# Performance work log

Hardware: AMD Instinct MI355X
Metric: run time of the kernel (lower is better)

The kernel has to match this reference:

```python
import jax, jax.numpy as jnp
import numpy as np

B, T, D = 16, 4096, 512
V = 512          # cif value dim
H_ALPHA = 128    # alpha_net hidden
N_MAX = 400      # static max target length (fill_max of target_lengths)
EPS = 1e-8


def _layernorm(x, g, b, eps=1e-5):
    mu = jnp.mean(x, axis=-1, keepdims=True)
    var = jnp.mean(jnp.square(x - mu), axis=-1, keepdims=True)
    return (x - mu) * jax.lax.rsqrt(var + eps) * g + b


def setup_inputs() -> dict:
    key = jax.random.key(0)
    ks = jax.random.split(key, 10)
    h = jax.random.normal(ks[0], (B, T, D), dtype=jnp.float32)
    target_lengths = jax.random.randint(ks[1], (B,), 1, N_MAX + 1)          # 1..400
    input_lengths = jax.random.randint(ks[2], (B,), T // 2, T + 1)          # 2048..4096
    s = 1.0 / np.sqrt(D)
    params = {
        "ln_g": jnp.ones((D,), jnp.float32),
        "ln_b": jnp.zeros((D,), jnp.float32),
        "W1": jax.random.normal(ks[3], (D, H_ALPHA), jnp.float32) * s,
        "b1": jnp.zeros((H_ALPHA,), jnp.float32),
        "W2": jax.random.normal(ks[4], (H_ALPHA, 1), jnp.float32) * (1.0 / np.sqrt(H_ALPHA)),
        "b2": jnp.zeros((1,), jnp.float32),
        "Wv": jax.random.normal(ks[5], (D, V), jnp.float32) * s,
        "bv": jnp.zeros((V,), jnp.float32),
    }
    return {"h": h, "target_lengths": target_lengths, "input_lengths": input_lengths, **params}


def reference(h, target_lengths, input_lengths, ln_g, ln_b, W1, b1, W2, b2, Wv, bv):
    dt = h.dtype
    # alpha_net: LayerNorm -> Linear -> SiLU -> Linear -> softplus -> [B,T]
    x = _layernorm(h, ln_g, ln_b)
    x = jax.nn.silu(x @ W1 + b1)
    raw_alpha = jax.nn.softplus((x @ W2 + b2)[..., 0])  # [B,T]

    # mask padding & rescale so sum_t alpha = N per sample
    mask = (jnp.arange(T)[None, :] < input_lengths[:, None]).astype(dt)  # [B,T]
    alpha = raw_alpha * mask
    sums = jnp.sum(alpha, axis=1)                       # [B]
    Nf = target_lengths.astype(dt)
    alpha_scaled = alpha * (Nf / (sums + EPS))[:, None]
    Lf = jnp.maximum(input_lengths.astype(dt), 1.0)
    alpha_uniform = mask * (Nf / Lf)[:, None]
    use_uniform = (sums < 10 * EPS).astype(dt)[:, None]
    alpha = alpha_scaled * (1.0 - use_uniform) + alpha_uniform * use_uniform

    v = h @ Wv + bv                                     # [B,T,V]

    # mass-space overlap: w[b,t,k] = clamp(min(c_t,k) - max(c_{t-1},k-1), 0)
    c = jnp.cumsum(alpha, axis=1)                       # [B,T]
    c_prev = c - alpha
    k = jnp.arange(1, N_MAX + 1, dtype=dt)[None, None, :]  # [1,1,N]
    left = jnp.maximum(c_prev[..., None], k - 1.0)
    right = jnp.minimum(c[..., None], k)
    w = jnp.clip(right - left, 0.0)                     # [B,T,N]

    token_mask = jnp.arange(N_MAX)[None, :] < target_lengths[:, None]  # [B,N] bool
    tokens = jnp.einsum('btn,btv->bnv', w, v)           # [B,N,V]
    cif_mass = jnp.sum(w, axis=1)                       # [B,N]
    frame_durations = jnp.sum(w / (alpha + EPS)[..., None], axis=1)    # [B,N]

    tm = token_mask.astype(dt)
    tokens = tokens * tm[..., None]
    cif_mass = cif_mass * tm
    frame_durations = frame_durations * tm
    return tokens, frame_durations, cif_mass, token_mask, alpha, raw_alpha
```

## Files before the change

kernel.cpp:

```cpp
#include <hip/hip_runtime.h>
#include <math.h>


#define T_LEN 4096
#define D_DIM 512
#define HID   128
#define N_MAX 400
#define B_SZ  16
#define EPSF  1e-8f

typedef __attribute__((ext_vector_type(8))) short bf16x8;
typedef __attribute__((ext_vector_type(4))) float f32x4;

__device__ __forceinline__ unsigned short f2bf(float x) {
    unsigned u = __float_as_uint(x);
    unsigned r = (u + 0x7FFFu + ((u >> 16) & 1u)) >> 16;
    return (unsigned short)r;
}
__device__ __forceinline__ float bf2f(unsigned short h) {
    return __uint_as_float(((unsigned)h) << 16);
}

__global__ __launch_bounds__(256) void transpose_split_kernel(
    const float* __restrict__ in, unsigned short* __restrict__ out_hi,
    unsigned short* __restrict__ out_lo, int K, int N)
{
    __shared__ float tile[64][65];
    const int tid = threadIdx.x;
    const int k0 = blockIdx.x * 64, n0 = blockIdx.y * 64;
    #pragma unroll
    for (int i = 0; i < 16; ++i) {
        int idx = tid + i * 256;
        tile[idx >> 6][idx & 63] = in[(size_t)(k0 + (idx >> 6)) * N + n0 + (idx & 63)];
    }
    __syncthreads();
    #pragma unroll
    for (int i = 0; i < 16; ++i) {
        int idx = tid + i * 256;
        int nr = idx >> 6, kc = idx & 63;
        float x = tile[kc][nr];
        unsigned short hi = f2bf(x);
        out_hi[(size_t)(n0 + nr) * K + k0 + kc] = hi;
        if (out_lo) out_lo[(size_t)(n0 + nr) * K + k0 + kc] = f2bf(x - bf2f(hi));
    }
}

__global__ __launch_bounds__(256) void alpha_net_kernel(
    const float* __restrict__ h,
    const float* __restrict__ ln_g, const float* __restrict__ ln_b,
    const unsigned short* __restrict__ W1t_hi, const unsigned short* __restrict__ W1t_lo,
    const float* __restrict__ b1,
    const float* __restrict__ W2,   const float* __restrict__ b2,
    float* __restrict__ raw_alpha)
{
    __shared__ char planes[32 * 2064];
    __shared__ float part2[2][2][16];
    const int tid  = threadIdx.x;
    const int row0 = blockIdx.x * 32;
    const int wave = tid >> 6;
    const int lane = tid & 63;

    const int c1 = lane * 4;
    const int c2 = 256 + lane * 4;
    float4 g1 = *(const float4*)&ln_g[c1];
    float4 g2 = *(const float4*)&ln_g[c2];
    float4 o1 = *(const float4*)&ln_b[c1];
    float4 o2 = *(const float4*)&ln_b[c2];
    float4 av[8], bv8[8];
    const int rbase8 = wave * 8;
    #pragma unroll
    for (int rr = 0; rr < 8; ++rr) {
        const float* hrow = h + (size_t)(row0 + rbase8 + rr) * D_DIM;
        float4 a  = *(const float4*)(hrow + c1);
        float4 bq = *(const float4*)(hrow + c2);
        float s  = a.x + a.y + a.z + a.w + bq.x + bq.y + bq.z + bq.w;
        float sq = a.x*a.x + a.y*a.y + a.z*a.z + a.w*a.w
                 + bq.x*bq.x + bq.y*bq.y + bq.z*bq.z + bq.w*bq.w;
        #pragma unroll
        for (int off = 32; off >= 1; off >>= 1) {
            s  += __shfl_xor(s,  off);
            sq += __shfl_xor(sq, off);
        }
        float mu  = s * (1.0f / 512.0f);
        float var = sq * (1.0f / 512.0f) - mu * mu;
        float inv = rsqrtf(var + 1e-5f);
        a.x  = (a.x  - mu) * inv * g1.x + o1.x;
        a.y  = (a.y  - mu) * inv * g1.y + o1.y;
        a.z  = (a.z  - mu) * inv * g1.z + o1.z;
        a.w  = (a.w  - mu) * inv * g1.w + o1.w;
        bq.x = (bq.x - mu) * inv * g2.x + o2.x;
        bq.y = (bq.y - mu) * inv * g2.y + o2.y;
        bq.z = (bq.z - mu) * inv * g2.z + o2.z;
        bq.w = (bq.w - mu) * inv * g2.w + o2.w;
        av[rr] = a; bv8[rr] = bq;
    }
    #pragma unroll
    for (int rr = 0; rr < 8; ++rr) {
        char* rb = planes + (rbase8 + rr) * 2064;
        float4 a = av[rr], bq = bv8[rr];
        ushort4 ha = make_ushort4(f2bf(a.x), f2bf(a.y), f2bf(a.z), f2bf(a.w));
        ushort4 hb = make_ushort4(f2bf(bq.x), f2bf(bq.y), f2bf(bq.z), f2bf(bq.w));
        ushort4 la = make_ushort4(f2bf(a.x - bf2f(ha.x)), f2bf(a.y - bf2f(ha.y)),
                                  f2bf(a.z - bf2f(ha.z)), f2bf(a.w - bf2f(ha.w)));
        ushort4 lb = make_ushort4(f2bf(bq.x - bf2f(hb.x)), f2bf(bq.y - bf2f(hb.y)),
                                  f2bf(bq.z - bf2f(hb.z)), f2bf(bq.w - bf2f(hb.w)));
        *(ushort4*)(rb + 2 * c1)        = ha;
        *(ushort4*)(rb + 2 * c2)        = hb;
        *(ushort4*)(rb + 1024 + 2 * c1) = la;
        *(ushort4*)(rb + 1024 + 2 * c2) = lb;
    }
    __syncthreads();

    const int rt = wave >> 1, ch = wave & 1;
    const int lr = lane & 15, lg = lane >> 4;
    const char* aBase = planes + (rt * 16 + lr) * 2064;
    f32x4 acc[4];
    #pragma unroll
    for (int nt = 0; nt < 4; ++nt) acc[nt] = (f32x4){0.f, 0.f, 0.f, 0.f};
    for (int ks = 0; ks < 16; ++ks) {
        const int cofs = (4 * ks + lg) * 16;
        bf16x8 ahi = *(const bf16x8*)(aBase + cofs);
        bf16x8 alo = *(const bf16x8*)(aBase + 1024 + cofs);
        const int kofs = ks * 32 + lg * 8;
        #pragma unroll
        for (int nt = 0; nt < 4; ++nt) {
            int n = ch * 64 + nt * 16 + lr;
            bf16x8 bhi = *(const bf16x8*)(W1t_hi + (size_t)n * D_DIM + kofs);
            bf16x8 blo = *(const bf16x8*)(W1t_lo + (size_t)n * D_DIM + kofs);
            acc[nt] = __builtin_amdgcn_mfma_f32_16x16x32_bf16(ahi, bhi, acc[nt], 0, 0, 0);
            acc[nt] = __builtin_amdgcn_mfma_f32_16x16x32_bf16(ahi, blo, acc[nt], 0, 0, 0);
            acc[nt] = __builtin_amdgcn_mfma_f32_16x16x32_bf16(alo, bhi, acc[nt], 0, 0, 0);
        }
    }

    float p[4] = {0.f, 0.f, 0.f, 0.f};
    #pragma unroll
    for (int nt = 0; nt < 4; ++nt) {
        int n = ch * 64 + nt * 16 + lr;
        float b1v = b1[n], w2v = W2[n];
        #pragma unroll
        for (int j = 0; j < 4; ++j) {
            float z = acc[nt][j] + b1v;
            p[j] += z / (1.f + expf(-z)) * w2v;
        }
    }
    #pragma unroll
    for (int j = 0; j < 4; ++j) {
        p[j] += __shfl_xor(p[j], 1);
        p[j] += __shfl_xor(p[j], 2);
        p[j] += __shfl_xor(p[j], 4);
        p[j] += __shfl_xor(p[j], 8);
    }
    if (lr == 0) {
        #pragma unroll
        for (int j = 0; j < 4; ++j) part2[ch][rt][lg * 4 + j] = p[j];
    }
    __syncthreads();
    if (tid < 32) {
        int r16 = tid & 15, rt2 = tid >> 4;
        float z = part2[0][rt2][r16] + part2[1][rt2][r16] + b2[0];
        float sp = fmaxf(z, 0.f) + log1pf(expf(-fabsf(z)));
        raw_alpha[row0 + rt2 * 16 + r16] = sp;
    }
}

__global__ __launch_bounds__(256) void chunk_sum_kernel(
    const float* __restrict__ raw, const int* __restrict__ ilen,
    float* __restrict__ S)
{
    __shared__ float wred[4];
    const int ch = blockIdx.x, b = blockIdx.y;
    const int tid = threadIdx.x;
    const int L = min(ilen[b], T_LEN);
    const int base = ch << 10;
    float local = 0.f;
    #pragma unroll
    for (int i = 0; i < 4; ++i) {
        int t = base + tid + (i << 8);
        if (t < L) local += raw[b * T_LEN + t];
    }
    #pragma unroll
    for (int off = 32; off >= 1; off >>= 1) local += __shfl_xor(local, off);
    if ((tid & 63) == 0) wred[tid >> 6] = local;
    __syncthreads();
    if (tid == 0) S[b * 4 + ch] = wred[0] + wred[1] + wred[2] + wred[3];
}

__global__ __launch_bounds__(1024) void scan_chunk_kernel(
    const float* __restrict__ raw, const float* __restrict__ S,
    const int* __restrict__ tgt, const int* __restrict__ ilen,
    float* __restrict__ alpha_out, float* __restrict__ c_out)
{
    __shared__ float wsum_lds[16];
    __shared__ float wscan_lds[16];
    const int ch = blockIdx.x, b = blockIdx.y;
    const int tid  = threadIdx.x;
    const int wid  = tid >> 6;
    const int lane = tid & 63;
    const int L    = min(ilen[b], T_LEN);
    const float Nf = (float)tgt[b];

    float s0 = S[b * 4 + 0], s1 = S[b * 4 + 1], s2 = S[b * 4 + 2], s3 = S[b * 4 + 3];
    float sums  = s0 + s1 + s2 + s3;
    float scale = Nf / (sums + EPSF);
    float uu    = (sums < 10.f * EPSF) ? 1.f : 0.f;
    float unif  = Nf / fmaxf((float)L, 1.f);
    float prefix = (ch > 0 ? s0 : 0.f) + (ch > 1 ? s1 : 0.f) + (ch > 2 ? s2 : 0.f);
    float carry  = (1.f - uu) * scale * prefix
                 + uu * unif * (float)min(L, ch << 10);

    int t = (ch << 10) + tid;
    float m = (t < L) ? 1.f : 0.f;
    float a = (raw[b * T_LEN + t] * m * scale) * (1.f - uu) + m * unif * uu;
    alpha_out[b * T_LEN + t] = a;

    float v = a;
    #pragma unroll
    for (int off = 1; off < 64; off <<= 1) {
        float tv = __shfl_up(v, off);
        if (lane >= off) v += tv;
    }
    if (lane == 63) wsum_lds[wid] = v;
    __syncthreads();
    if (wid == 0 && lane < 16) {
        float s = wsum_lds[lane];
        #pragma unroll
        for (int off = 1; off < 16; off <<= 1) {
            float tv = __shfl_up(s, off);
            if (lane >= off) s += tv;
        }
        wscan_lds[lane] = s;
    }
    __syncthreads();
    float woff = (wid > 0) ? wscan_lds[wid - 1] : 0.f;
    c_out[b * T_LEN + t] = carry + woff + v;
}

__global__ __launch_bounds__(256) void cif_gather_kernel(
    const float* __restrict__ h, const float* __restrict__ alpha,
    const float* __restrict__ c_arr,
    const int* __restrict__ tgt, const int* __restrict__ ilen,
    unsigned short* __restrict__ hwb, float* __restrict__ fd_out,
    float* __restrict__ cm_out, float* __restrict__ tm_out)
{
    __shared__ float part[514];
    const int n   = blockIdx.x;
    const int b   = blockIdx.y;
    const int tid = threadIdx.x;
    const int oidx = b * N_MAX + n;
    if (n >= tgt[b]) {
        if (tid == 0) { fd_out[oidx] = 0.f; cm_out[oidx] = 0.f; tm_out[oidx] = 0.f; }
        return;
    }
    const int L = min(ilen[b], T_LEN);
    const float* cb = c_arr + b * T_LEN;
    const float* ab = alpha + b * T_LEN;
    const float nf  = (float)n;
    const float nf1 = nf + 1.0f;

    int lo = 0, hi = T_LEN;
    while (lo < hi) { int mid = (lo + hi) >> 1; if (cb[mid] > nf) hi = mid; else lo = mid + 1; }
    const int t0 = lo;
    lo = 0; hi = T_LEN;
    while (lo < hi) { int mid = (lo + hi) >> 1; if (cb[mid] >= nf1) hi = mid; else lo = mid + 1; }
    int t1 = min(lo, L - 1);

    const int par = tid >> 7;
    const int c4  = (tid & 127) << 2;
    float4 acc = make_float4(0.f, 0.f, 0.f, 0.f);
    float wsum = 0.f, fdsum = 0.f;
    const float* hb = h + (size_t)(b * T_LEN) * D_DIM;
    for (int t = t0 + par; t <= t1; t += 2) {
        float a = ab[t], c = cb[t];
        float cp = c - a;
        float w  = fmaxf(fminf(c, nf1) - fmaxf(cp, nf), 0.f);
        wsum  += w;
        fdsum += w / (a + EPSF);
        const float4 hv = *(const float4*)(hb + (size_t)t * D_DIM + c4);
        acc.x += w * hv.x;
        acc.y += w * hv.y;
        acc.z += w * hv.z;
        acc.w += w * hv.w;
    }
    if (par == 1) {
        *(float4*)&part[c4] = acc;
        if (tid == 128) { part[512] = wsum; part[513] = fdsum; }
    }
    __syncthreads();
    if (par == 0) {
        float4 p = *(const float4*)&part[c4];
        acc.x += p.x; acc.y += p.y; acc.z += p.z; acc.w += p.w;
        *(ushort4*)(hwb + (size_t)oidx * D_DIM + c4) =
            make_ushort4(f2bf(acc.x), f2bf(acc.y), f2bf(acc.z), f2bf(acc.w));
        if (tid == 0) {
            fd_out[oidx] = fdsum + part[513];
            cm_out[oidx] = wsum + part[512];
            tm_out[oidx] = 1.f;
        }
    }
}

__global__ __launch_bounds__(256) void token_gemm_kernel(
    const unsigned short* __restrict__ hwb, const unsigned short* __restrict__ Wvt,
    const float* __restrict__ bv, const float* __restrict__ cm,
    const int* __restrict__ tgt, float* __restrict__ tokens)
{
    const int tid  = threadIdx.x;
    const int wave = tid >> 6;
    const int lane = tid & 63;
    const int lr = lane & 15, lg = lane >> 4;
    const int arow = blockIdx.x * 64 + wave * 16 + lr;
    const int colb = blockIdx.y * 128;

    f32x4 acc[8];
    #pragma unroll
    for (int nt = 0; nt < 8; ++nt) acc[nt] = (f32x4){0.f, 0.f, 0.f, 0.f};
    for (int ks = 0; ks < 16; ++ks) {
        const int kofs = ks * 32 + lg * 8;
        bf16x8 a = *(const bf16x8*)(hwb + (size_t)arow * D_DIM + kofs);
        #pragma unroll
        for (int nt = 0; nt < 8; ++nt) {
            int n = colb + nt * 16 + lr;
            bf16x8 bq = *(const bf16x8*)(Wvt + (size_t)n * D_DIM + kofs);
            acc[nt] = __builtin_amdgcn_mfma_f32_16x16x32_bf16(a, bq, acc[nt], 0, 0, 0);
        }
    }

    float cmr[4], mr[4];
    int   rr[4];
    #pragma unroll
    for (int j = 0; j < 4; ++j) {
        int r = blockIdx.x * 64 + wave * 16 + lg * 4 + j;
        int bb = r / N_MAX;
        int nn = r - bb * N_MAX;
        rr[j] = r;
        mr[j] = (nn < tgt[bb]) ? 1.f : 0.f;
        cmr[j] = cm[r];
    }
    #pragma unroll
    for (int nt = 0; nt < 8; ++nt) {
        int col = colb + nt * 16 + lr;
        float bvv = bv[col];
        #pragma unroll
        for (int j = 0; j < 4; ++j)
            tokens[(size_t)rr[j] * D_DIM + col] = mr[j] * (acc[nt][j] + cmr[j] * bvv);
    }
}

extern "C" void kernel_launch(void* const* d_in, const int* in_sizes, int n_in,
                              void* d_out, int out_size, void* d_ws, size_t ws_size,
                              hipStream_t stream)
{
    (void)in_sizes; (void)n_in; (void)out_size; (void)ws_size;
    const float* h    = (const float*)d_in[0];
    const int*   tgt  = (const int*)  d_in[1];
    const int*   ilen = (const int*)  d_in[2];
    const float* lng  = (const float*)d_in[3];
    const float* lnb  = (const float*)d_in[4];
    const float* W1   = (const float*)d_in[5];
    const float* b1   = (const float*)d_in[6];
    const float* W2   = (const float*)d_in[7];
    const float* b2   = (const float*)d_in[8];
    const float* Wv   = (const float*)d_in[9];
    const float* bv   = (const float*)d_in[10];

    float* out    = (float*)d_out;
    float* tokens = out;
    float* fd     = tokens + (size_t)B_SZ * N_MAX * D_DIM;
    float* cm     = fd + B_SZ * N_MAX;
    float* tm     = cm + B_SZ * N_MAX;
    float* alpha  = tm + B_SZ * N_MAX;
    float* raw    = alpha + B_SZ * T_LEN;

    float* c_ws = (float*)d_ws;
    unsigned short* hwb    = (unsigned short*)(c_ws + B_SZ * T_LEN);
    unsigned short* W1t_hi = hwb + (size_t)B_SZ * N_MAX * D_DIM;
    unsigned short* W1t_lo = W1t_hi + (size_t)HID * D_DIM;
    unsigned short* Wvt    = W1t_lo + (size_t)HID * D_DIM;
    float* S = (float*)(Wvt + (size_t)D_DIM * D_DIM);

    transpose_split_kernel<<<dim3(8, 2), 256, 0, stream>>>(W1, W1t_hi, W1t_lo, D_DIM, HID);
    transpose_split_kernel<<<dim3(8, 8), 256, 0, stream>>>(Wv, Wvt, (unsigned short*)nullptr,
                                                           D_DIM, D_DIM);
    alpha_net_kernel<<<(B_SZ * T_LEN) / 32, 256, 0, stream>>>(h, lng, lnb, W1t_hi, W1t_lo,
                                                              b1, W2, b2, raw);
    chunk_sum_kernel<<<dim3(4, B_SZ), 256, 0, stream>>>(raw, ilen, S);
    scan_chunk_kernel<<<dim3(4, B_SZ), 1024, 0, stream>>>(raw, S, tgt, ilen, alpha, c_ws);
    cif_gather_kernel<<<dim3(N_MAX, B_SZ), 256, 0, stream>>>(h, alpha, c_ws, tgt, ilen,
                                                             hwb, fd, cm, tm);
    token_gemm_kernel<<<dim3(100, 4), 256, 0, stream>>>(hwb, Wvt, bv, cm, tgt, tokens);
}
```

Before: 410.3 us.

## Pack weights into MFMA fragment order and rebalance alpha-net wave tiling

Replaces the shared-memory weight transpose with a kernel that writes W1 and Wv directly in per-lane MFMA fragment order, so each wave's B-operand load becomes one contiguous 16-byte-per-lane access. In alpha_net, each wave now computes both 16-row tiles over 32 hidden columns instead of one row tile over 64 columns. This halves how much weight data each wave reads and reuses the A fragments held in registers. The layernorm and bf16-split stores are also fused into a single loop, dropping the register arrays. The pack kernel reads the weights with strided global loads, but it runs only once per call on small matrices.

```diff
diff --git a/kernel.cpp b/kernel.cpp
--- a/kernel.cpp
+++ b/kernel.cpp
@@ -21,40 +21,45 @@
     return __uint_as_float(((unsigned)h) << 16);
 }
 
-__global__ __launch_bounds__(256) void transpose_split_kernel(
+__global__ __launch_bounds__(256) void frag_pack_kernel(
     const float* __restrict__ in, unsigned short* __restrict__ out_hi,
     unsigned short* __restrict__ out_lo, int K, int N)
 {
-    __shared__ float tile[64][65];
-    const int tid = threadIdx.x;
-    const int k0 = blockIdx.x * 64, n0 = blockIdx.y * 64;
-    #pragma unroll
-    for (int i = 0; i < 16; ++i) {
-        int idx = tid + i * 256;
-        tile[idx >> 6][idx & 63] = in[(size_t)(k0 + (idx >> 6)) * N + n0 + (idx & 63)];
-    }
-    __syncthreads();
-    #pragma unroll
-    for (int i = 0; i < 16; ++i) {
-        int idx = tid + i * 256;
-        int nr = idx >> 6, kc = idx & 63;
-        float x = tile[kc][nr];
+    const int idx = blockIdx.x * 256 + threadIdx.x;
+    const int nks = K >> 5;
+    const int total = (N >> 4) * nks * 64;
+    if (idx >= total) return;
+    const int lane = idx & 63;
+    const int ks   = (idx >> 6) % nks;
+    const int ntg  = idx / (nks << 6);
+    const int n  = ntg * 16 + (lane & 15);
+    const int k0 = ks * 32 + (lane >> 4) * 8;
+    unsigned short hv[8], lv[8];
+    #pragma unroll
+    for (int e = 0; e < 8; ++e) {
+        float x = in[(size_t)(k0 + e) * N + n];
         unsigned short hi = f2bf(x);
-        out_hi[(size_t)(n0 + nr) * K + k0 + kc] = hi;
-        if (out_lo) out_lo[(size_t)(n0 + nr) * K + k0 + kc] = f2bf(x - bf2f(hi));
+        hv[e] = hi;
+        lv[e] = f2bf(x - bf2f(hi));
+    }
+    *(ushort4*)(out_hi + (size_t)idx * 8)     = make_ushort4(hv[0], hv[1], hv[2], hv[3]);
+    *(ushort4*)(out_hi + (size_t)idx * 8 + 4) = make_ushort4(hv[4], hv[5], hv[6], hv[7]);
+    if (out_lo) {
+        *(ushort4*)(out_lo + (size_t)idx * 8)     = make_ushort4(lv[0], lv[1], lv[2], lv[3]);
+        *(ushort4*)(out_lo + (size_t)idx * 8 + 4) = make_ushort4(lv[4], lv[5], lv[6], lv[7]);
     }
 }
 
 __global__ __launch_bounds__(256) void alpha_net_kernel(
     const float* __restrict__ h,
     const float* __restrict__ ln_g, const float* __restrict__ ln_b,
-    const unsigned short* __restrict__ W1t_hi, const unsigned short* __restrict__ W1t_lo,
+    const unsigned short* __restrict__ W1f_hi, const unsigned short* __restrict__ W1f_lo,
     const float* __restrict__ b1,
     const float* __restrict__ W2,   const float* __restrict__ b2,
     float* __restrict__ raw_alpha)
 {
     __shared__ char planes[32 * 2064];
-    __shared__ float part2[2][2][16];
+    __shared__ float part2[4][2][16];
     const int tid  = threadIdx.x;
     const int row0 = blockIdx.x * 32;
     const int wave = tid >> 6;
@@ -66,7 +71,6 @@
     float4 g2 = *(const float4*)&ln_g[c2];
     float4 o1 = *(const float4*)&ln_b[c1];
     float4 o2 = *(const float4*)&ln_b[c2];
-    float4 av[8], bv8[8];
     const int rbase8 = wave * 8;
     #pragma unroll
     for (int rr = 0; rr < 8; ++rr) {
@@ -92,12 +96,7 @@
         bq.y = (bq.y - mu) * inv * g2.y + o2.y;
         bq.z = (bq.z - mu) * inv * g2.z + o2.z;
         bq.w = (bq.w - mu) * inv * g2.w + o2.w;
-        av[rr] = a; bv8[rr] = bq;
-    }
-    #pragma unroll
-    for (int rr = 0; rr < 8; ++rr) {
         char* rb = planes + (rbase8 + rr) * 2064;
-        float4 a = av[rr], bq = bv8[rr];
         ushort4 ha = make_ushort4(f2bf(a.x), f2bf(a.y), f2bf(a.z), f2bf(a.w));
         ushort4 hb = make_ushort4(f2bf(bq.x), f2bf(bq.y), f2bf(bq.z), f2bf(bq.w));
         ushort4 la = make_ushort4(f2bf(a.x - bf2f(ha.x)), f2bf(a.y - bf2f(ha.y)),
@@ -111,54 +110,67 @@
     }
     __syncthreads();
 
-    const int rt = wave >> 1, ch = wave & 1;
     const int lr = lane & 15, lg = lane >> 4;
-    const char* aBase = planes + (rt * 16 + lr) * 2064;
-    f32x4 acc[4];
-    #pragma unroll
-    for (int nt = 0; nt < 4; ++nt) acc[nt] = (f32x4){0.f, 0.f, 0.f, 0.f};
+    const char* aBase0 = planes + lr * 2064;
+    const char* aBase1 = planes + (16 + lr) * 2064;
+    f32x4 acc[2][2];
+    #pragma unroll
+    for (int rt = 0; rt < 2; ++rt)
+        #pragma unroll
+        for (int nt = 0; nt < 2; ++nt) acc[rt][nt] = (f32x4){0.f, 0.f, 0.f, 0.f};
     for (int ks = 0; ks < 16; ++ks) {
         const int cofs = (4 * ks + lg) * 16;
-        bf16x8 ahi = *(const bf16x8*)(aBase + cofs);
-        bf16x8 alo = *(const bf16x8*)(aBase + 1024 + cofs);
-        const int kofs = ks * 32 + lg * 8;
-        #pragma unroll
-        for (int nt = 0; nt < 4; ++nt) {
-            int n = ch * 64 + nt * 16 + lr;
-            bf16x8 bhi = *(const bf16x8*)(W1t_hi + (size_t)n * D_DIM + kofs);
-            bf16x8 blo = *(const bf16x8*)(W1t_lo + (size_t)n * D_DIM + kofs);
-            acc[nt] = __builtin_amdgcn_mfma_f32_16x16x32_bf16(ahi, bhi, acc[nt], 0, 0, 0);
-            acc[nt] = __builtin_amdgcn_mfma_f32_16x16x32_bf16(ahi, blo, acc[nt], 0, 0, 0);
-            acc[nt] = __builtin_amdgcn_mfma_f32_16x16x32_bf16(alo, bhi, acc[nt], 0, 0, 0);
-        }
-    }
-
-    float p[4] = {0.f, 0.f, 0.f, 0.f};
-    #pragma unroll
-    for (int nt = 0; nt < 4; ++nt) {
-        int n = ch * 64 + nt * 16 + lr;
+        bf16x8 ahi0 = *(const bf16x8*)(aBase0 + cofs);
+        bf16x8 alo0 = *(const bf16x8*)(aBase0 + 1024 + cofs);
+        bf16x8 ahi1 = *(const bf16x8*)(aBase1 + cofs);
+        bf16x8 alo1 = *(const bf16x8*)(aBase1 + 1024 + cofs);
+        #pragma unroll
+        for (int nt = 0; nt < 2; ++nt) {
+            const size_t fo = ((size_t)((wave * 2 + nt) * 16 + ks) * 64 + lane) * 8;
+            bf16x8 bhi = *(const bf16x8*)(W1f_hi + fo);
+            bf16x8 blo = *(const bf16x8*)(W1f_lo + fo);
+            acc[0][nt] = __builtin_amdgcn_mfma_f32_16x16x32_bf16(ahi0, bhi, acc[0][nt], 0, 0, 0);
+            acc[0][nt] = __builtin_amdgcn_mfma_f32_16x16x32_bf16(ahi0, blo, acc[0][nt], 0, 0, 0);
+            acc[0][nt] = __builtin_amdgcn_mfma_f32_16x16x32_bf16(alo0, bhi, acc[0][nt], 0, 0, 0);
+            acc[1][nt] = __builtin_amdgcn_mfma_f32_16x16x32_bf16(ahi1, bhi, acc[1][nt], 0, 0, 0);
+            acc[1][nt] = __builtin_amdgcn_mfma_f32_16x16x32_bf16(ahi1, blo, acc[1][nt], 0, 0, 0);
+            acc[1][nt] = __builtin_amdgcn_mfma_f32_16x16x32_bf16(alo1, bhi, acc[1][nt], 0, 0, 0);
+        }
+    }
+
+    float p[2][4] = {};
+    #pragma unroll
+    for (int nt = 0; nt < 2; ++nt) {
+        int n = (wave * 2 + nt) * 16 + lr;
         float b1v = b1[n], w2v = W2[n];
         #pragma unroll
+        for (int rt = 0; rt < 2; ++rt)
+            #pragma unroll
+            for (int j = 0; j < 4; ++j) {
+                float z = acc[rt][nt][j] + b1v;
+                p[rt][j] += z / (1.f + expf(-z)) * w2v;
+            }
+    }
+    #pragma unroll
+    for (int rt = 0; rt < 2; ++rt)
+        #pragma unroll
         for (int j = 0; j < 4; ++j) {
-            float z = acc[nt][j] + b1v;
-            p[j] += z / (1.f + expf(-z)) * w2v;
-        }
-    }
-    #pragma unroll
-    for (int j = 0; j < 4; ++j) {
-        p[j] += __shfl_xor(p[j], 1);
-        p[j] += __shfl_xor(p[j], 2);
-        p[j] += __shfl_xor(p[j], 4);
-        p[j] += __shfl_xor(p[j], 8);
-    }
+            p[rt][j] += __shfl_xor(p[rt][j], 1);
+            p[rt][j] += __shfl_xor(p[rt][j], 2);
+            p[rt][j] += __shfl_xor(p[rt][j], 4);
+            p[rt][j] += __shfl_xor(p[rt][j], 8);
+        }
     if (lr == 0) {
         #pragma unroll
-        for (int j = 0; j < 4; ++j) part2[ch][rt][lg * 4 + j] = p[j];
+        for (int rt = 0; rt < 2; ++rt)
+            #pragma unroll
+            for (int j = 0; j < 4; ++j) part2[wave][rt][lg * 4 + j] = p[rt][j];
     }
     __syncthreads();
     if (tid < 32) {
         int r16 = tid & 15, rt2 = tid >> 4;
-        float z = part2[0][rt2][r16] + part2[1][rt2][r16] + b2[0];
+        float z = part2[0][rt2][r16] + part2[1][rt2][r16]
+                + part2[2][rt2][r16] + part2[3][rt2][r16] + b2[0];
         float sp = fmaxf(z, 0.f) + log1pf(expf(-fabsf(z)));
         raw_alpha[row0 + rt2 * 16 + r16] = sp;
     }
@@ -301,7 +313,7 @@
 }
 
 __global__ __launch_bounds__(256) void token_gemm_kernel(
-    const unsigned short* __restrict__ hwb, const unsigned short* __restrict__ Wvt,
+    const unsigned short* __restrict__ hwb, const unsigned short* __restrict__ Wvf,
     const float* __restrict__ bv, const float* __restrict__ cm,
     const int* __restrict__ tgt, float* __restrict__ tokens)
 {
@@ -320,8 +332,8 @@
         bf16x8 a = *(const bf16x8*)(hwb + (size_t)arow * D_DIM + kofs);
         #pragma unroll
         for (int nt = 0; nt < 8; ++nt) {
-            int n = colb + nt * 16 + lr;
-            bf16x8 bq = *(const bf16x8*)(Wvt + (size_t)n * D_DIM + kofs);
+            const int ntg = blockIdx.y * 8 + nt;
+            bf16x8 bq = *(const bf16x8*)(Wvf + ((size_t)(ntg * 16 + ks) * 64 + lane) * 8);
             acc[nt] = __builtin_amdgcn_mfma_f32_16x16x32_bf16(a, bq, acc[nt], 0, 0, 0);
         }
     }
@@ -374,19 +386,18 @@
 
     float* c_ws = (float*)d_ws;
     unsigned short* hwb    = (unsigned short*)(c_ws + B_SZ * T_LEN);
-    unsigned short* W1t_hi = hwb + (size_t)B_SZ * N_MAX * D_DIM;
-    unsigned short* W1t_lo = W1t_hi + (size_t)HID * D_DIM;
-    unsigned short* Wvt    = W1t_lo + (size_t)HID * D_DIM;
-    float* S = (float*)(Wvt + (size_t)D_DIM * D_DIM);
-
-    transpose_split_kernel<<<dim3(8, 2), 256, 0, stream>>>(W1, W1t_hi, W1t_lo, D_DIM, HID);
-    transpose_split_kernel<<<dim3(8, 8), 256, 0, stream>>>(Wv, Wvt, (unsigned short*)nullptr,
-                                                           D_DIM, D_DIM);
-    alpha_net_kernel<<<(B_SZ * T_LEN) / 32, 256, 0, stream>>>(h, lng, lnb, W1t_hi, W1t_lo,
+    unsigned short* W1f_hi = hwb + (size_t)B_SZ * N_MAX * D_DIM;
+    unsigned short* W1f_lo = W1f_hi + (size_t)HID * D_DIM;
+    unsigned short* Wvf    = W1f_lo + (size_t)HID * D_DIM;
+    float* S = (float*)(Wvf + (size_t)D_DIM * D_DIM);
+
+    frag_pack_kernel<<<32, 256, 0, stream>>>(W1, W1f_hi, W1f_lo, D_DIM, HID);
+    frag_pack_kernel<<<128, 256, 0, stream>>>(Wv, Wvf, (unsigned short*)nullptr, D_DIM, D_DIM);
+    alpha_net_kernel<<<(B_SZ * T_LEN) / 32, 256, 0, stream>>>(h, lng, lnb, W1f_hi, W1f_lo,
                                                               b1, W2, b2, raw);
     chunk_sum_kernel<<<dim3(4, B_SZ), 256, 0, stream>>>(raw, ilen, S);
     scan_chunk_kernel<<<dim3(4, B_SZ), 1024, 0, stream>>>(raw, S, tgt, ilen, alpha, c_ws);
     cif_gather_kernel<<<dim3(N_MAX, B_SZ), 256, 0, stream>>>(h, alpha, c_ws, tgt, ilen,
                                                              hwb, fd, cm, tm);
-    token_gemm_kernel<<<dim3(100, 4), 256, 0, stream>>>(hwb, Wvt, bv, cm, tgt, tokens);
-}
+    token_gemm_kernel<<<dim3(100, 4), 256, 0, stream>>>(hwb, Wvf, bv, cm, tgt, tokens);
+}
```

Measured after the change: 331.4 us. 19.2% less time.
